# Kernel tuning notes

Hardware: AMD Instinct MI355X
Metric: run time of the kernel (lower is better)

Reference implementation:

```python
import jax, jax.numpy as jnp
import numpy as np

MAX_VISIT = 200
NUM_CODE = 506          # feature vocab -> 507 multi-hot dims
NUM_TGT = 284           # target vocab multi-hot dims
B = 64
P = 40                  # codes per visit
D_OTH = 57              # others feature dim (sign slice [37:] is 20-dim)
K = 100                 # len(weight_idx)
LSTM = 256
D_FEAT = (NUM_CODE + 1) + K + 27 + (D_OTH - 37)   # 654
D_FWD = D_FEAT + 10                                # 664
D_MLP_IN = (NUM_CODE + 1) + (D_OTH - 37) + 20 + 8  # 555


def multi_hot(codes, n):
    """Binary multi-hot encode int codes over last axis. codes: [..., P]."""
    shp = codes.shape
    flat = codes.reshape(-1, shp[-1])
    R = flat.shape[0]
    rows = jnp.repeat(jnp.arange(R), shp[-1])
    z = jnp.zeros((R, n), jnp.float32).at[rows, flat.reshape(-1)].set(1.0)
    return z.reshape(shp[:-1] + (n,))


def reverse_sequence(x, lengths):
    """tf.reverse_sequence along axis 1: reverse first lengths[i] steps, keep rest."""
    T = x.shape[1]
    j = jnp.arange(T)[None, :]
    L = lengths[:, None]
    idx = jnp.where(j < L, L - 1 - j, j)          # [B, T]
    return jnp.take_along_axis(x, idx[:, :, None], axis=1)


def setup_inputs() -> dict:
    key = jax.random.key(0)
    ks = jax.random.split(key, 13)
    code = jax.random.randint(ks[0], (B, MAX_VISIT, P), 0, NUM_CODE + 1, dtype=jnp.int32)
    others = jax.random.normal(ks[1], (B, MAX_VISIT, D_OTH), jnp.float32)
    length = jax.random.randint(ks[2], (B,), 3, MAX_VISIT + 1, dtype=jnp.int32)
    target = jax.random.randint(ks[3], (B, 10), 0, NUM_TGT, dtype=jnp.int32)
    weight_idx = jax.random.randint(ks[4], (K,), 0, NUM_TGT, dtype=jnp.int32)
    s = 0.02
    Wf = jax.random.normal(ks[5], (D_FWD, LSTM), jnp.float32) * s
    bf = jnp.zeros((LSTM,), jnp.float32)
    Wb = jax.random.normal(ks[6], (D_FWD, LSTM), jnp.float32) * s
    bb = jnp.zeros((LSTM,), jnp.float32)
    W0 = jax.random.normal(ks[7], (D_MLP_IN, 256), jnp.float32) * s
    b0 = jnp.zeros((256,), jnp.float32)
    W1 = jax.random.normal(ks[8], (256, 256), jnp.float32) * s
    b1 = jnp.zeros((256,), jnp.float32)
    return {"code": code, "others": others, "length": length, "target": target,
            "weight_idx": weight_idx, "Wf": Wf, "bf": bf, "Wb": Wb, "bb": bb,
            "W0": W0, "b0": b0, "W1": W1, "b1": b1}


def reference(code, others, length, target, weight_idx, Wf, bf, Wb, bb, W0, b0, W1, b1):
    code_mh = multi_hot(code, NUM_CODE + 1)                      # [B,200,507]
    # valid-visit mask (dense analogue of tf.boolean_mask over [B,198])
    mask = (jnp.arange(MAX_VISIT - 2)[None, :] < (length - 2)[:, None]).astype(jnp.float32)
    sign = others[:, 1:-1, 37:]                                  # [B,198,20]
    interval_ = jnp.concatenate([others[:, 1:-1, 27:37], others[:, 2:, 27:37]], axis=-1)
    stay = others[:, 1:-1, 19:27]
    x = jnp.concatenate([code_mh[:, 1:-1], sign, interval_, stay], axis=-1)  # [B,198,555]
    h = jax.nn.relu(x @ W0 + b0) @ W1 + b1                       # [B,198,256]
    fv = h / jnp.sqrt(jnp.sum(h * h, axis=-1, keepdims=True))
    fv = fv * mask[:, :, None]                                   # zero invalid rows
    # target block: gather (1 - multi-hot) at weight_idx, tile over visits
    tgt = 1.0 - multi_hot(target, NUM_TGT)                       # [B,284]
    tgt = tgt[:, weight_idx]                                     # [B,K]
    tgt = jnp.broadcast_to(tgt[:, None, :], (B, MAX_VISIT, K))
    code_full = jnp.concatenate([code_mh, tgt], axis=-1)         # [B,200,607]
    interval = others[:, :, 27:37]
    interval_backward = jnp.concatenate(
        [jnp.zeros((B, 1, 10), jnp.float32), reverse_sequence(interval, length)[:, :-1]], axis=1)
    feature = jnp.concatenate([code_full, others[:, :, :27], others[:, :, 37:]], axis=-1)
    feature_backward = reverse_sequence(feature, length)
    x_forward = jnp.concatenate([feature, interval], axis=-1)[:, :-2] @ Wf + bf
    x_backward = jnp.concatenate([feature_backward, interval_backward], axis=-1)[:, :-2] @ Wb + bb
    return (x_forward, x_backward, fv)
```

## Files before the change

### kernel.cpp

```cpp
#include <hip/hip_runtime.h>
#include <hip/hip_bf16.h>

typedef unsigned short u16;
typedef __attribute__((ext_vector_type(8))) short short8;
typedef __attribute__((ext_vector_type(4))) float f32x4;

#define TMAX 200
#define TOUT 198
#define PC 40
#define DOTH 57
#define NKT 9
#define FWD_OFF 0
#define BWD_OFF 3244032
#define FV_OFF  6488064
#define OWF 0
#define OWB 294912
#define OW0 589824
#define OW1 884736
#define OTF 1015808
#define OTB 1081344
#define WS_BYTES 1146880

__device__ __align__(16) unsigned char g_ws[WS_BYTES];

__device__ __forceinline__ u16 f2b(float v) {
  __hip_bfloat16 h = __float2bfloat16(v);
  return *(u16*)&h;
}

__global__ __launch_bounds__(256) void prep_kernel(
    const int* __restrict__ target, const int* __restrict__ widx,
    const float* __restrict__ Wf, const float* __restrict__ bfv,
    const float* __restrict__ Wb, const float* __restrict__ bbv,
    const float* __restrict__ W0, const float* __restrict__ W1)
{
  u16*   wsu = (u16*)g_ws;
  float* wsf = (float*)g_ws;
  int blk = blockIdx.x, n = threadIdx.x;
  if (blk < 248) {
    const float* src; u16* dst; int kb; int mode;
    if (blk < 72)       { src=Wf; dst=wsu+OWF/2; kb=blk;     mode=0; }
    else if (blk < 144) { src=Wb; dst=wsu+OWB/2; kb=blk-72;  mode=0; }
    else if (blk < 216) { src=W0; dst=wsu+OW0/2; kb=blk-144; mode=1; }
    else                { src=W1; dst=wsu+OW1/2; kb=blk-216; mode=2; }
    u16 pk[8];
    #pragma unroll
    for (int j=0;j<8;j++) {
      int k = kb*8+j;
      int sr;
      if (mode==0)      sr = (k<57)? 607+k : (k<564)? k-57 : -1;
      else if (mode==1) sr = (k<48)? 507+k : (k<57)? -1 : (k<564)? k-57 : -1;
      else              sr = k;
      float v = (sr>=0)? src[sr*256+n] : 0.f;
      pk[j] = f2b(v);
    }
    *(uint4*)(dst + (kb*256+n)*8) = *(uint4*)pk;
  } else {
    int b = blk - 248;
    __shared__ float tval[100]; __shared__ int tg[10];
    if (n<10) tg[n]=target[b*10+n];
    __syncthreads();
    if (n<100){ int w=widx[n]; float v=1.f;
      #pragma unroll
      for(int i=0;i<10;i++) if(tg[i]==w) v=0.f;
      tval[n]=v; }
    __syncthreads();
    float aF=bfv[n], aB=bbv[n];
    for(int k=0;k<100;k++){ float v=tval[k];
      aF=fmaf(v,Wf[(507+k)*256+n],aF); aB=fmaf(v,Wb[(507+k)*256+n],aB); }
    wsf[OTF/4 + b*256+n]=aF; wsf[OTB/4 + b*256+n]=aB;
  }
}

__global__ __launch_bounds__(256) void gemm_kernel(
    const int* __restrict__ code, const float* __restrict__ others,
    const int* __restrict__ length,
    const float* __restrict__ b0, const float* __restrict__ b1,
    float* __restrict__ out)
{
  const u16*   wsu = (const u16*)g_ws;
  const float* wsf = (const float*)g_ws;
  const int tile = blockIdx.x;
  const int strm = blockIdx.y;
  const int tid = threadIdx.x;
  const int wv = tid>>6, lane = tid&63, q = lane>>4, c = lane&15;
  const int colbase = wv*64 + c;

  __shared__ u16 lA[NKT*2048];
  __shared__ int rowB[32], rowT[32], rowS[32], rowS2[32], rowL[32];
  __shared__ float rpart[4][32];
  __shared__ int s_skip;

  if (tid == 0) s_skip = 1;
  if (tid < 32) {
    int m = tile*32 + tid;
    int b = m/198, t = m - b*198;
    int L = length[b];
    int s, s2 = 0;
    if (strm==0) s = t;
    else if (strm==1){ s = (t<L)? (L-1-t) : t;
                       s2 = (t==0)? -1 : (((t-1)<L)? (L-t) : (t-1)); }
    else s = t+1;
    rowB[tid]=b; rowT[tid]=t; rowS[tid]=s; rowS2[tid]=s2; rowL[tid]=L;
  }
  __syncthreads();

  if (strm == 2) {
    if (tid < 32 && rowT[tid] < rowL[tid]-2) s_skip = 0;
    __syncthreads();
    if (s_skip) {
      f32x4 z = {0.f, 0.f, 0.f, 0.f};
      #pragma unroll
      for (int it=0; it<8; it++) {
        int lin = it*256 + tid;
        int r = lin>>6, c4 = (lin&63)<<2;
        *(f32x4*)(out + FV_OFF + (rowB[r]*TOUT + rowT[r])*256 + c4) = z;
      }
      return;
    }
  }

  int myp[5], myr[5];
  #pragma unroll
  for (int it=0; it<5; it++) {
    int idx = tid + it*256;
    int r = idx/40, p = idx - r*40;
    myr[it] = r*8;
    myp[it] = 57 + code[(rowB[r]*TMAX + rowS[r])*PC + p];
  }

  float dv[8];
  if (strm < 2) {
    #pragma unroll
    for (int it=0; it<8; it++) {
      int idx = tid + it*256;
      float v = 0.f;
      if (idx < 32*57) {
        int r = idx/57, j = idx - r*57;
        int col = (j<27)? j : (j<47)? 37+(j-27) : 27+(j-47);
        int sr = (strm==1 && j>=47)? rowS2[r] : rowS[r];
        if (sr >= 0) v = others[(rowB[r]*TMAX + sr)*DOTH + col];
      }
      dv[it] = v;
    }
  } else {
    #pragma unroll
    for (int it=0; it<6; it++) {
      int idx = tid + it*256;
      int r = idx/48, j = idx - r*48;
      int t = rowT[r], srow, col;
      if (j<20)      { srow=t+1; col=37+j; }
      else if (j<30) { srow=t+1; col=27+(j-20); }
      else if (j<40) { srow=t+2; col=27+(j-30); }
      else           { srow=t+1; col=19+(j-40); }
      dv[it] = others[(rowB[r]*TMAX + srow)*DOTH + col];
    }
  }

  f32x4 acc[2][4];
  if (strm < 2) {
    const float* tg = wsf + ((strm==0)? OTF/4 : OTB/4);
    #pragma unroll
    for (int mt=0; mt<2; mt++)
      #pragma unroll
      for (int reg=0; reg<4; reg++) {
        int rl = mt*16 + q*4 + reg;
        const float* tr = tg + rowB[rl]*256;
        #pragma unroll
        for (int nt=0; nt<4; nt++) acc[mt][nt][reg] = tr[colbase + nt*16];
      }
  } else {
    #pragma unroll
    for (int nt=0; nt<4; nt++){ float v = b0[colbase + nt*16];
      #pragma unroll
      for (int mt=0; mt<2; mt++)
        #pragma unroll
        for (int reg=0; reg<4; reg++) acc[mt][nt][reg]=v; }
  }

  const u16* Wpk = wsu + ((strm==0)? OWF/2 : (strm==1)? OWB/2 : OW0/2);
  short8 bb[2][8];
  {
    const u16* gB0 = Wpk + ((q    )*256 + colbase)*8;
    const u16* gB1 = Wpk + ((4 + q)*256 + colbase)*8;
    #pragma unroll
    for (int nt=0; nt<4; nt++) {
      bb[0][nt]   = *(const short8*)(gB0 + nt*128);
      bb[0][nt+4] = *(const short8*)(gB1 + nt*128);
    }
  }

  { uint4 z = {0,0,0,0};
    #pragma unroll
    for (int i=0; i<NKT; i++) ((uint4*)lA)[tid + i*256] = z;
  }
  __syncthreads();
  #pragma unroll
  for (int it=0; it<5; it++) {
    int d = myp[it];
    lA[(d>>3)*256 + myr[it] + (d&7)] = 0x3F80;
  }
  if (strm < 2) {
    #pragma unroll
    for (int it=0; it<8; it++) {
      int idx = tid + it*256;
      if (idx < 32*57) {
        int r = idx/57, j = idx - r*57;
        lA[(j>>3)*256 + r*8 + (j&7)] = f2b(dv[it]);
      }
    }
  } else {
    #pragma unroll
    for (int it=0; it<6; it++) {
      int idx = tid + it*256;
      int r = idx/48, j = idx - r*48;
      lA[(j>>3)*256 + r*8 + (j&7)] = f2b(dv[it]);
    }
  }
  __syncthreads();

  #pragma unroll
  for (int kt=0; kt<NKT; kt++) {
    const u16* A = lA + kt*2048;
    short8 af0[2], af1[2];
    #pragma unroll
    for (int mt=0; mt<2; mt++) af0[mt] = *(const short8*)&A[(q    )*256 + (mt*16 + c)*8];
    #pragma unroll
    for (int mt=0; mt<2; mt++) af1[mt] = *(const short8*)&A[(4 + q)*256 + (mt*16 + c)*8];
    if (kt < NKT-1) {
      const u16* gB0 = Wpk + (((kt+1)*8 + q    )*256 + colbase)*8;
      const u16* gB1 = Wpk + (((kt+1)*8 + 4 + q)*256 + colbase)*8;
      #pragma unroll
      for (int nt=0; nt<4; nt++) {
        bb[(kt+1)&1][nt]   = *(const short8*)(gB0 + nt*128);
        bb[(kt+1)&1][nt+4] = *(const short8*)(gB1 + nt*128);
      }
    }
    #pragma unroll
    for (int mt=0; mt<2; mt++)
      #pragma unroll
      for (int nt=0; nt<4; nt++)
        acc[mt][nt] = __builtin_amdgcn_mfma_f32_16x16x32_bf16(af0[mt], bb[kt&1][nt], acc[mt][nt], 0,0,0);
    #pragma unroll
    for (int mt=0; mt<2; mt++)
      #pragma unroll
      for (int nt=0; nt<4; nt++)
        acc[mt][nt] = __builtin_amdgcn_mfma_f32_16x16x32_bf16(af1[mt], bb[kt&1][nt+4], acc[mt][nt], 0,0,0);
  }

  if (strm < 2) {
    float* o = out + ((strm==0)? FWD_OFF : BWD_OFF);
    #pragma unroll
    for (int mt=0; mt<2; mt++)
      #pragma unroll
      for (int reg=0; reg<4; reg++) {
        int rl = mt*16 + q*4 + reg;
        float* orow = o + (rowB[rl]*TOUT + rowT[rl])*256 + colbase;
        #pragma unroll
        for (int nt=0; nt<4; nt++) orow[nt*16] = acc[mt][nt][reg];
      }
  } else {
    __syncthreads();
    if (wv == 0) {
      #pragma unroll
      for (int mt=0; mt<2; mt++)
        #pragma unroll
        for (int reg=0; reg<4; reg++) {
          int rl = mt*16 + q*4 + reg;
          #pragma unroll
          for (int nt=0; nt<4; nt++) {
            int kl = c + nt*16;
            lA[(kl>>3)*256 + rl*8 + (kl&7)] = f2b(fmaxf(acc[mt][nt][reg], 0.f));
          }
        }
    }
    const u16* W1p = wsu + OW1/2;
    short8 bw[2][4];
    {
      const u16* gB = W1p + ((q)*256 + colbase)*8;
      #pragma unroll
      for (int nt=0; nt<4; nt++) bw[0][nt] = *(const short8*)(gB + nt*128);
    }
    __syncthreads();
    f32x4 a2[2][4];
    #pragma unroll
    for (int nt=0; nt<4; nt++){ float v = b1[colbase + nt*16];
      #pragma unroll
      for (int mt=0; mt<2; mt++)
        #pragma unroll
        for (int reg=0; reg<4; reg++) a2[mt][nt][reg]=v; }
    #pragma unroll
    for (int kt2=0; kt2<4; kt2++) {
      if (wv == kt2+1) {
        u16* B2 = lA + ((kt2+1)&1)*2048;
        #pragma unroll
        for (int mt=0; mt<2; mt++)
          #pragma unroll
          for (int reg=0; reg<4; reg++) {
            int rl = mt*16 + q*4 + reg;
            #pragma unroll
            for (int nt=0; nt<4; nt++) {
              int kl = c + nt*16;
              B2[(kl>>3)*256 + rl*8 + (kl&7)] = f2b(fmaxf(acc[mt][nt][reg], 0.f));
            }
          }
      }
      #pragma unroll
      for (int s=0; s<2; s++) {
        const int step = kt2*2 + s;
        const u16* A2 = lA + (kt2&1)*2048;
        int akb = s*4 + q;
        short8 af[2];
        #pragma unroll
        for (int mt=0; mt<2; mt++) af[mt] = *(const short8*)&A2[akb*256 + (mt*16 + c)*8];
        if (step < 7) {
          const int nstep = step + 1;
          const u16* gB = W1p + (((nstep>>1)*8 + (nstep&1)*4 + q)*256 + colbase)*8;
          #pragma unroll
          for (int nt=0; nt<4; nt++) bw[nstep&1][nt] = *(const short8*)(gB + nt*128);
        }
        #pragma unroll
        for (int mt=0; mt<2; mt++)
          #pragma unroll
          for (int nt=0; nt<4; nt++)
            a2[mt][nt] = __builtin_amdgcn_mfma_f32_16x16x32_bf16(af[mt], bw[step&1][nt], a2[mt][nt], 0,0,0);
      }
      __syncthreads();
    }
    #pragma unroll
    for (int mt=0; mt<2; mt++)
      #pragma unroll
      for (int reg=0; reg<4; reg++) {
        int rl = mt*16 + q*4 + reg;
        float ss = 0.f;
        #pragma unroll
        for (int nt=0; nt<4; nt++){ float v=a2[mt][nt][reg]; ss = fmaf(v,v,ss); }
        ss += __shfl_xor(ss, 1, 64); ss += __shfl_xor(ss, 2, 64);
        ss += __shfl_xor(ss, 4, 64); ss += __shfl_xor(ss, 8, 64);
        if (c==0) rpart[wv][rl] = ss;
      }
    __syncthreads();
    #pragma unroll
    for (int mt=0; mt<2; mt++)
      #pragma unroll
      for (int reg=0; reg<4; reg++) {
        int rl = mt*16 + q*4 + reg;
        float s = rpart[0][rl]+rpart[1][rl]+rpart[2][rl]+rpart[3][rl];
        float inv = (s>0.f)? (1.0f/sqrtf(s)) : 0.f;
        int t = rowT[rl];
        if (t >= rowL[rl]-2) inv = 0.f;
        float* orow = out + FV_OFF + (rowB[rl]*TOUT + t)*256 + colbase;
        #pragma unroll
        for (int nt=0; nt<4; nt++) orow[nt*16] = a2[mt][nt][reg]*inv;
      }
  }
}

extern "C" void kernel_launch(void* const* d_in, const int* in_sizes, int n_in,
                              void* d_out, int out_size, void* d_ws, size_t ws_size,
                              hipStream_t stream) {
  const int*   code    = (const int*)d_in[0];
  const float* others  = (const float*)d_in[1];
  const int*   length  = (const int*)d_in[2];
  const int*   target  = (const int*)d_in[3];
  const int*   widx    = (const int*)d_in[4];
  const float* Wf      = (const float*)d_in[5];
  const float* bfv     = (const float*)d_in[6];
  const float* Wb      = (const float*)d_in[7];
  const float* bbv     = (const float*)d_in[8];
  const float* W0      = (const float*)d_in[9];
  const float* b0v     = (const float*)d_in[10];
  const float* W1      = (const float*)d_in[11];
  const float* b1v     = (const float*)d_in[12];
  (void)d_ws; (void)ws_size;

  float* out = (float*)d_out;

  prep_kernel<<<dim3(312), dim3(256), 0, stream>>>(target, widx, Wf, bfv, Wb, bbv, W0, W1);
  gemm_kernel<<<dim3(396,3), dim3(256), 0, stream>>>(code, others, length, b0v, b1v, out);
}
```

Baseline: 124.6 us.

## Stage output tiles through LDS for vectorized stores and simplify MLP second layer

Accumulator outputs are first written to a padded LDS tile and then stored to global memory as contiguous 16-byte vectors, replacing scattered scalar stores. The second MLP layer now has every wave write its ReLU slice to LDS up front, followed by a plain non-unrolled K loop, instead of interleaving staged writes with barriers. Register double-buffering of weight prefetches is removed in favour of loads inside a non-unrolled loop, and launch bounds now request 4 blocks per CU. The goal is higher occupancy and store coalescing, at the cost of less explicit latency hiding for global weight loads and extra LDS round trips and barriers.

```diff
diff --git a/kernel.cpp b/kernel.cpp
--- a/kernel.cpp
+++ b/kernel.cpp
@@ -72,7 +72,7 @@
   }
 }
 
-__global__ __launch_bounds__(256) void gemm_kernel(
+__global__ __launch_bounds__(256, 4) void gemm_kernel(
     const int* __restrict__ code, const float* __restrict__ others,
     const int* __restrict__ length,
     const float* __restrict__ b0, const float* __restrict__ b1,
@@ -86,7 +86,7 @@
   const int wv = tid>>6, lane = tid&63, q = lane>>4, c = lane&15;
   const int colbase = wv*64 + c;
 
-  __shared__ u16 lA[NKT*2048];
+  __shared__ __align__(16) u16 lA[NKT*2048];
   __shared__ int rowB[32], rowT[32], rowS[32], rowS2[32], rowL[32];
   __shared__ float rpart[4][32];
   __shared__ int s_skip;
@@ -178,21 +178,9 @@
         for (int reg=0; reg<4; reg++) acc[mt][nt][reg]=v; }
   }
 
-  const u16* Wpk = wsu + ((strm==0)? OWF/2 : (strm==1)? OWB/2 : OW0/2);
-  short8 bb[2][8];
-  {
-    const u16* gB0 = Wpk + ((q    )*256 + colbase)*8;
-    const u16* gB1 = Wpk + ((4 + q)*256 + colbase)*8;
-    #pragma unroll
-    for (int nt=0; nt<4; nt++) {
-      bb[0][nt]   = *(const short8*)(gB0 + nt*128);
-      bb[0][nt+4] = *(const short8*)(gB1 + nt*128);
-    }
-  }
-
   { uint4 z = {0,0,0,0};
     #pragma unroll
-    for (int i=0; i<NKT; i++) ((uint4*)lA)[tid + i*256] = z;
+    for (int i=0; i<9; i++) ((uint4*)lA)[tid + i*256] = z;
   }
   __syncthreads();
   #pragma unroll
@@ -219,49 +207,58 @@
   }
   __syncthreads();
 
-  #pragma unroll
+  const u16* Wpk = wsu + ((strm==0)? OWF/2 : (strm==1)? OWB/2 : OW0/2);
+  #pragma unroll 1
   for (int kt=0; kt<NKT; kt++) {
+    const u16* gB0 = Wpk + ((kt*8 + q    )*256 + colbase)*8;
+    const u16* gB1 = Wpk + ((kt*8 + 4 + q)*256 + colbase)*8;
+    short8 bb[8];
+    #pragma unroll
+    for (int nt=0; nt<4; nt++) {
+      bb[nt]   = *(const short8*)(gB0 + nt*128);
+      bb[nt+4] = *(const short8*)(gB1 + nt*128);
+    }
     const u16* A = lA + kt*2048;
     short8 af0[2], af1[2];
     #pragma unroll
     for (int mt=0; mt<2; mt++) af0[mt] = *(const short8*)&A[(q    )*256 + (mt*16 + c)*8];
     #pragma unroll
     for (int mt=0; mt<2; mt++) af1[mt] = *(const short8*)&A[(4 + q)*256 + (mt*16 + c)*8];
-    if (kt < NKT-1) {
-      const u16* gB0 = Wpk + (((kt+1)*8 + q    )*256 + colbase)*8;
-      const u16* gB1 = Wpk + (((kt+1)*8 + 4 + q)*256 + colbase)*8;
-      #pragma unroll
-      for (int nt=0; nt<4; nt++) {
-        bb[(kt+1)&1][nt]   = *(const short8*)(gB0 + nt*128);
-        bb[(kt+1)&1][nt+4] = *(const short8*)(gB1 + nt*128);
-      }
-    }
     #pragma unroll
     for (int mt=0; mt<2; mt++)
       #pragma unroll
       for (int nt=0; nt<4; nt++)
-        acc[mt][nt] = __builtin_amdgcn_mfma_f32_16x16x32_bf16(af0[mt], bb[kt&1][nt], acc[mt][nt], 0,0,0);
+        acc[mt][nt] = __builtin_amdgcn_mfma_f32_16x16x32_bf16(af0[mt], bb[nt], acc[mt][nt], 0,0,0);
     #pragma unroll
     for (int mt=0; mt<2; mt++)
       #pragma unroll
       for (int nt=0; nt<4; nt++)
-        acc[mt][nt] = __builtin_amdgcn_mfma_f32_16x16x32_bf16(af1[mt], bb[kt&1][nt+4], acc[mt][nt], 0,0,0);
+        acc[mt][nt] = __builtin_amdgcn_mfma_f32_16x16x32_bf16(af1[mt], bb[nt+4], acc[mt][nt], 0,0,0);
   }
 
   if (strm < 2) {
-    float* o = out + ((strm==0)? FWD_OFF : BWD_OFF);
+    __syncthreads();
+    float* fC = (float*)lA;
     #pragma unroll
     for (int mt=0; mt<2; mt++)
       #pragma unroll
       for (int reg=0; reg<4; reg++) {
         int rl = mt*16 + q*4 + reg;
-        float* orow = o + (rowB[rl]*TOUT + rowT[rl])*256 + colbase;
-        #pragma unroll
-        for (int nt=0; nt<4; nt++) orow[nt*16] = acc[mt][nt][reg];
-      }
-  } else {
-    __syncthreads();
-    if (wv == 0) {
+        #pragma unroll
+        for (int nt=0; nt<4; nt++) fC[rl*260 + colbase + nt*16] = acc[mt][nt][reg];
+      }
+    __syncthreads();
+    float* o = out + ((strm==0)? FWD_OFF : BWD_OFF);
+    #pragma unroll
+    for (int it=0; it<8; it++) {
+      int row = it*4 + (tid>>6), col = (tid&63)*4;
+      f32x4 v = *(f32x4*)&fC[row*260 + col];
+      *(f32x4*)(o + (rowB[row]*TOUT + rowT[row])*256 + col) = v;
+    }
+  } else {
+    __syncthreads();
+    {
+      u16* B2 = lA + wv*2048;
       #pragma unroll
       for (int mt=0; mt<2; mt++)
         #pragma unroll
@@ -270,62 +267,36 @@
           #pragma unroll
           for (int nt=0; nt<4; nt++) {
             int kl = c + nt*16;
-            lA[(kl>>3)*256 + rl*8 + (kl&7)] = f2b(fmaxf(acc[mt][nt][reg], 0.f));
+            B2[(kl>>3)*256 + rl*8 + (kl&7)] = f2b(fmaxf(acc[mt][nt][reg], 0.f));
           }
         }
     }
+    __syncthreads();
+    f32x4 a2[2][4];
+    #pragma unroll
+    for (int nt=0; nt<4; nt++){ float v = b1[colbase + nt*16];
+      #pragma unroll
+      for (int mt=0; mt<2; mt++)
+        #pragma unroll
+        for (int reg=0; reg<4; reg++) a2[mt][nt][reg]=v; }
     const u16* W1p = wsu + OW1/2;
-    short8 bw[2][4];
-    {
-      const u16* gB = W1p + ((q)*256 + colbase)*8;
-      #pragma unroll
-      for (int nt=0; nt<4; nt++) bw[0][nt] = *(const short8*)(gB + nt*128);
-    }
-    __syncthreads();
-    f32x4 a2[2][4];
-    #pragma unroll
-    for (int nt=0; nt<4; nt++){ float v = b1[colbase + nt*16];
+    #pragma unroll 1
+    for (int step=0; step<8; step++) {
+      int kt2 = step>>1;
+      int akb = (step&1)*4 + q;
+      const u16* gB = W1p + ((kt2*8 + akb)*256 + colbase)*8;
+      short8 bf[4];
+      #pragma unroll
+      for (int nt=0; nt<4; nt++) bf[nt] = *(const short8*)(gB + nt*128);
+      const u16* A2 = lA + kt2*2048;
+      short8 af[2];
+      #pragma unroll
+      for (int mt=0; mt<2; mt++) af[mt] = *(const short8*)&A2[akb*256 + (mt*16 + c)*8];
       #pragma unroll
       for (int mt=0; mt<2; mt++)
         #pragma unroll
-        for (int reg=0; reg<4; reg++) a2[mt][nt][reg]=v; }
-    #pragma unroll
-    for (int kt2=0; kt2<4; kt2++) {
-      if (wv == kt2+1) {
-        u16* B2 = lA + ((kt2+1)&1)*2048;
-        #pragma unroll
-        for (int mt=0; mt<2; mt++)
-          #pragma unroll
-          for (int reg=0; reg<4; reg++) {
-            int rl = mt*16 + q*4 + reg;
-            #pragma unroll
-            for (int nt=0; nt<4; nt++) {
-              int kl = c + nt*16;
-              B2[(kl>>3)*256 + rl*8 + (kl&7)] = f2b(fmaxf(acc[mt][nt][reg], 0.f));
-            }
-          }
-      }
-      #pragma unroll
-      for (int s=0; s<2; s++) {
-        const int step = kt2*2 + s;
-        const u16* A2 = lA + (kt2&1)*2048;
-        int akb = s*4 + q;
-        short8 af[2];
-        #pragma unroll
-        for (int mt=0; mt<2; mt++) af[mt] = *(const short8*)&A2[akb*256 + (mt*16 + c)*8];
-        if (step < 7) {
-          const int nstep = step + 1;
-          const u16* gB = W1p + (((nstep>>1)*8 + (nstep&1)*4 + q)*256 + colbase)*8;
-          #pragma unroll
-          for (int nt=0; nt<4; nt++) bw[nstep&1][nt] = *(const short8*)(gB + nt*128);
-        }
-        #pragma unroll
-        for (int mt=0; mt<2; mt++)
-          #pragma unroll
-          for (int nt=0; nt<4; nt++)
-            a2[mt][nt] = __builtin_amdgcn_mfma_f32_16x16x32_bf16(af[mt], bw[step&1][nt], a2[mt][nt], 0,0,0);
-      }
-      __syncthreads();
+        for (int nt=0; nt<4; nt++)
+          a2[mt][nt] = __builtin_amdgcn_mfma_f32_16x16x32_bf16(af[mt], bf[nt], a2[mt][nt], 0,0,0);
     }
     #pragma unroll
     for (int mt=0; mt<2; mt++)
@@ -340,6 +311,7 @@
         if (c==0) rpart[wv][rl] = ss;
       }
     __syncthreads();
+    float* fC = (float*)lA;
     #pragma unroll
     for (int mt=0; mt<2; mt++)
       #pragma unroll
@@ -347,12 +319,17 @@
         int rl = mt*16 + q*4 + reg;
         float s = rpart[0][rl]+rpart[1][rl]+rpart[2][rl]+rpart[3][rl];
         float inv = (s>0.f)? (1.0f/sqrtf(s)) : 0.f;
-        int t = rowT[rl];
-        if (t >= rowL[rl]-2) inv = 0.f;
-        float* orow = out + FV_OFF + (rowB[rl]*TOUT + t)*256 + colbase;
-        #pragma unroll
-        for (int nt=0; nt<4; nt++) orow[nt*16] = a2[mt][nt][reg]*inv;
-      }
+        if (rowT[rl] >= rowL[rl]-2) inv = 0.f;
+        #pragma unroll
+        for (int nt=0; nt<4; nt++) fC[rl*260 + colbase + nt*16] = a2[mt][nt][reg]*inv;
+      }
+    __syncthreads();
+    #pragma unroll
+    for (int it=0; it<8; it++) {
+      int row = it*4 + (tid>>6), col = (tid&63)*4;
+      f32x4 v = *(f32x4*)&fC[row*260 + col];
+      *(f32x4*)(out + FV_OFF + (rowB[row]*TOUT + rowT[row])*256 + col) = v;
+    }
   }
 }
 
```

Result: no change. 122.9 us (-1.4%).

## Retile LSTM-input GEMM to 64x128 blocks with rolling 3-slot LDS A buffer

Applied to the files above, without the earlier changes.

The forward/backward projection GEMMs now use 64-row by 128-column tiles (grid 198x2x3) instead of 32-row by full-width tiles. The A operand is built per 64-wide K chunk in a rotating three-buffer LDS ring rather than materialising all nine K tiles up front. The MLP stream keeps 32-row tiles, chosen by the half index, and uses the same rolling buffer. The goal is to shrink LDS usage for higher occupancy (launch_bounds 256,3) and to overlap zeroing and scattering of the multi-hot A with the MFMAs, at the cost of a barrier per K step and fewer weight columns reused per block.

```diff
diff --git a/kernel.cpp b/kernel.cpp
--- a/kernel.cpp
+++ b/kernel.cpp
@@ -66,13 +66,14 @@
       tval[n]=v; }
     __syncthreads();
     float aF=bfv[n], aB=bbv[n];
+    #pragma unroll 4
     for(int k=0;k<100;k++){ float v=tval[k];
       aF=fmaf(v,Wf[(507+k)*256+n],aF); aB=fmaf(v,Wb[(507+k)*256+n],aB); }
     wsf[OTF/4 + b*256+n]=aF; wsf[OTB/4 + b*256+n]=aB;
   }
 }
 
-__global__ __launch_bounds__(256) void gemm_kernel(
+__global__ __launch_bounds__(256, 3) void gemm_kernel(
     const int* __restrict__ code, const float* __restrict__ others,
     const int* __restrict__ length,
     const float* __restrict__ b0, const float* __restrict__ b1,
@@ -81,19 +82,19 @@
   const u16*   wsu = (const u16*)g_ws;
   const float* wsf = (const float*)g_ws;
   const int tile = blockIdx.x;
-  const int strm = blockIdx.y;
+  const int half = blockIdx.y;
+  const int strm = blockIdx.z;
   const int tid = threadIdx.x;
   const int wv = tid>>6, lane = tid&63, q = lane>>4, c = lane&15;
-  const int colbase = wv*64 + c;
-
-  __shared__ u16 lA[NKT*2048];
-  __shared__ int rowB[32], rowT[32], rowS[32], rowS2[32], rowL[32];
-  __shared__ float rpart[4][32];
+
+  __shared__ __align__(16) u16 lA[3][4096];
+  __shared__ int rowB[64], rowT[64], rowS[64], rowS2[64], rowL[64];
+  __shared__ float rpart[4][64];
   __shared__ int s_skip;
 
   if (tid == 0) s_skip = 1;
-  if (tid < 32) {
-    int m = tile*32 + tid;
+  if (tid < 64) {
+    int m = tile*64 + tid;
     int b = m/198, t = m - b*198;
     int L = length[b];
     int s, s2 = 0;
@@ -105,37 +106,24 @@
   }
   __syncthreads();
 
-  if (strm == 2) {
-    if (tid < 32 && rowT[tid] < rowL[tid]-2) s_skip = 0;
-    __syncthreads();
-    if (s_skip) {
-      f32x4 z = {0.f, 0.f, 0.f, 0.f};
-      #pragma unroll
-      for (int it=0; it<8; it++) {
-        int lin = it*256 + tid;
-        int r = lin>>6, c4 = (lin&63)<<2;
-        *(f32x4*)(out + FV_OFF + (rowB[r]*TOUT + rowT[r])*256 + c4) = z;
-      }
-      return;
-    }
-  }
-
-  int myp[5], myr[5];
-  #pragma unroll
-  for (int it=0; it<5; it++) {
-    int idx = tid + it*256;
-    int r = idx/40, p = idx - r*40;
-    myr[it] = r*8;
-    myp[it] = 57 + code[(rowB[r]*TMAX + rowS[r])*PC + p];
-  }
-
-  float dv[8];
   if (strm < 2) {
-    #pragma unroll
-    for (int it=0; it<8; it++) {
+    const int colbase = half*128 + wv*32 + c;
+
+    int myp[10], myr[10];
+    #pragma unroll
+    for (int it=0; it<10; it++) {
+      int idx = tid + it*256;
+      int r = idx/40, p = idx - r*40;
+      myr[it] = r*8;
+      myp[it] = 57 + code[(rowB[r]*TMAX + rowS[r])*PC + p];
+    }
+
+    float dv[15];
+    #pragma unroll
+    for (int it=0; it<15; it++) {
       int idx = tid + it*256;
       float v = 0.f;
-      if (idx < 32*57) {
+      if (idx < 3648) {
         int r = idx/57, j = idx - r*57;
         int col = (j<27)? j : (j<47)? 37+(j-27) : 27+(j-47);
         int sr = (strm==1 && j>=47)? rowS2[r] : rowS[r];
@@ -143,124 +131,216 @@
       }
       dv[it] = v;
     }
+
+    f32x4 acc[4][2];
+    {
+      const float* tg = wsf + ((strm==0)? OTF/4 : OTB/4);
+      #pragma unroll
+      for (int mt=0; mt<4; mt++)
+        #pragma unroll
+        for (int reg=0; reg<4; reg++) {
+          int rl = mt*16 + q*4 + reg;
+          const float* tr = tg + rowB[rl]*256;
+          #pragma unroll
+          for (int nt=0; nt<2; nt++) acc[mt][nt][reg] = tr[colbase + nt*16];
+        }
+    }
+
+    const u16* Wpk = wsu + ((strm==0)? OWF/2 : OWB/2);
+    short8 bb[2][4];
+    #pragma unroll
+    for (int kb=0; kb<2; kb++) {
+      const u16* gB = Wpk + ((kb*4 + q)*256 + colbase)*8;
+      #pragma unroll
+      for (int nt=0; nt<2; nt++) bb[0][kb*2+nt] = *(const short8*)(gB + nt*128);
+    }
+
+    { uint4 z = {0,0,0,0};
+      ((uint4*)lA[0])[tid] = z; ((uint4*)lA[0])[tid+256] = z;
+      ((uint4*)lA[1])[tid] = z; ((uint4*)lA[1])[tid+256] = z; }
+    __syncthreads();
+    #pragma unroll
+    for (int it=0; it<10; it++) {
+      unsigned d = (unsigned)(myp[it]);
+      if (d < 64u) lA[0][(d>>3)*512 + myr[it] + (d&7)] = 0x3F80;
+    }
+    #pragma unroll
+    for (int it=0; it<15; it++) {
+      int idx = tid + it*256;
+      if (idx < 3648) {
+        int r = idx/57, j = idx - r*57;
+        lA[0][(j>>3)*512 + r*8 + (j&7)] = f2b(dv[it]);
+      }
+    }
+    __syncthreads();
+
+    #pragma unroll
+    for (int kt=0; kt<NKT; kt++) {
+      const u16* A = lA[kt%3];
+      short8 af0[4], af1[4];
+      #pragma unroll
+      for (int mt=0; mt<4; mt++) af0[mt] = *(const short8*)&A[(q    )*512 + (mt*16 + c)*8];
+      #pragma unroll
+      for (int mt=0; mt<4; mt++) af1[mt] = *(const short8*)&A[(4 + q)*512 + (mt*16 + c)*8];
+      if (kt < NKT-1) {
+        #pragma unroll
+        for (int kb=0; kb<2; kb++) {
+          const u16* gB = Wpk + (((kt+1)*8 + kb*4 + q)*256 + colbase)*8;
+          #pragma unroll
+          for (int nt=0; nt<2; nt++) bb[(kt+1)&1][kb*2+nt] = *(const short8*)(gB + nt*128);
+        }
+        u16* nb = lA[(kt+1)%3];
+        const int k0n = (kt+1)*64;
+        #pragma unroll
+        for (int it=0; it<10; it++) {
+          unsigned d = (unsigned)(myp[it] - k0n);
+          if (d < 64u) nb[(d>>3)*512 + myr[it] + (d&7)] = 0x3F80;
+        }
+      }
+      if (kt < NKT-2) {
+        uint4 z = {0,0,0,0};
+        ((uint4*)lA[(kt+2)%3])[tid] = z; ((uint4*)lA[(kt+2)%3])[tid+256] = z;
+      }
+      #pragma unroll
+      for (int mt=0; mt<4; mt++)
+        #pragma unroll
+        for (int nt=0; nt<2; nt++)
+          acc[mt][nt] = __builtin_amdgcn_mfma_f32_16x16x32_bf16(af0[mt], bb[kt&1][nt], acc[mt][nt], 0,0,0);
+      #pragma unroll
+      for (int mt=0; mt<4; mt++)
+        #pragma unroll
+        for (int nt=0; nt<2; nt++)
+          acc[mt][nt] = __builtin_amdgcn_mfma_f32_16x16x32_bf16(af1[mt], bb[kt&1][2+nt], acc[mt][nt], 0,0,0);
+      __syncthreads();
+    }
+
+    float* o = out + ((strm==0)? FWD_OFF : BWD_OFF);
+    #pragma unroll
+    for (int mt=0; mt<4; mt++)
+      #pragma unroll
+      for (int reg=0; reg<4; reg++) {
+        int rl = mt*16 + q*4 + reg;
+        float* orow = o + (rowB[rl]*TOUT + rowT[rl])*256 + colbase;
+        #pragma unroll
+        for (int nt=0; nt<2; nt++) orow[nt*16] = acc[mt][nt][reg];
+      }
   } else {
+    const int mo = half*32;
+    const int colbase = wv*64 + c;
+    u16* w32 = (u16*)lA;
+
+    if (tid < 32 && rowT[mo+tid] < rowL[mo+tid]-2) s_skip = 0;
+    __syncthreads();
+    if (s_skip) {
+      f32x4 z = {0.f, 0.f, 0.f, 0.f};
+      #pragma unroll
+      for (int it=0; it<8; it++) {
+        int lin = it*256 + tid;
+        int r = mo + (lin>>6), c4 = (lin&63)<<2;
+        *(f32x4*)(out + FV_OFF + (rowB[r]*TOUT + rowT[r])*256 + c4) = z;
+      }
+      return;
+    }
+
+    int myp[5], myr[5];
+    #pragma unroll
+    for (int it=0; it<5; it++) {
+      int idx = tid + it*256;
+      int r = idx/40, p = idx - r*40;
+      myr[it] = r*8;
+      myp[it] = 57 + code[(rowB[mo+r]*TMAX + rowS[mo+r])*PC + p];
+    }
+
+    float dv[6];
     #pragma unroll
     for (int it=0; it<6; it++) {
       int idx = tid + it*256;
       int r = idx/48, j = idx - r*48;
-      int t = rowT[r], srow, col;
+      int t = rowT[mo+r], srow, col;
       if (j<20)      { srow=t+1; col=37+j; }
       else if (j<30) { srow=t+1; col=27+(j-20); }
       else if (j<40) { srow=t+2; col=27+(j-30); }
       else           { srow=t+1; col=19+(j-40); }
-      dv[it] = others[(rowB[r]*TMAX + srow)*DOTH + col];
-    }
-  }
-
-  f32x4 acc[2][4];
-  if (strm < 2) {
-    const float* tg = wsf + ((strm==0)? OTF/4 : OTB/4);
-    #pragma unroll
-    for (int mt=0; mt<2; mt++)
-      #pragma unroll
-      for (int reg=0; reg<4; reg++) {
-        int rl = mt*16 + q*4 + reg;
-        const float* tr = tg + rowB[rl]*256;
-        #pragma unroll
-        for (int nt=0; nt<4; nt++) acc[mt][nt][reg] = tr[colbase + nt*16];
-      }
-  } else {
+      dv[it] = others[(rowB[mo+r]*TMAX + srow)*DOTH + col];
+    }
+
+    f32x4 acc[2][4];
     #pragma unroll
     for (int nt=0; nt<4; nt++){ float v = b0[colbase + nt*16];
       #pragma unroll
       for (int mt=0; mt<2; mt++)
         #pragma unroll
         for (int reg=0; reg<4; reg++) acc[mt][nt][reg]=v; }
-  }
-
-  const u16* Wpk = wsu + ((strm==0)? OWF/2 : (strm==1)? OWB/2 : OW0/2);
-  short8 bb[2][8];
-  {
-    const u16* gB0 = Wpk + ((q    )*256 + colbase)*8;
-    const u16* gB1 = Wpk + ((4 + q)*256 + colbase)*8;
-    #pragma unroll
-    for (int nt=0; nt<4; nt++) {
-      bb[0][nt]   = *(const short8*)(gB0 + nt*128);
-      bb[0][nt+4] = *(const short8*)(gB1 + nt*128);
-    }
-  }
-
-  { uint4 z = {0,0,0,0};
-    #pragma unroll
-    for (int i=0; i<NKT; i++) ((uint4*)lA)[tid + i*256] = z;
-  }
-  __syncthreads();
-  #pragma unroll
-  for (int it=0; it<5; it++) {
-    int d = myp[it];
-    lA[(d>>3)*256 + myr[it] + (d&7)] = 0x3F80;
-  }
-  if (strm < 2) {
-    #pragma unroll
-    for (int it=0; it<8; it++) {
-      int idx = tid + it*256;
-      if (idx < 32*57) {
-        int r = idx/57, j = idx - r*57;
-        lA[(j>>3)*256 + r*8 + (j&7)] = f2b(dv[it]);
-      }
-    }
-  } else {
+
+    const u16* Wpk = wsu + OW0/2;
+    short8 bb[2][8];
+    {
+      const u16* gB0 = Wpk + ((q    )*256 + colbase)*8;
+      const u16* gB1 = Wpk + ((4 + q)*256 + colbase)*8;
+      #pragma unroll
+      for (int nt=0; nt<4; nt++) {
+        bb[0][nt]   = *(const short8*)(gB0 + nt*128);
+        bb[0][nt+4] = *(const short8*)(gB1 + nt*128);
+      }
+    }
+
+    { uint4 z = {0,0,0,0};
+      ((uint4*)w32)[tid] = z; ((uint4*)w32)[tid+256] = z; }
+    __syncthreads();
+    #pragma unroll
+    for (int it=0; it<5; it++) {
+      unsigned d = (unsigned)(myp[it]);
+      if (d < 64u) w32[(d>>3)*256 + myr[it] + (d&7)] = 0x3F80;
+    }
     #pragma unroll
     for (int it=0; it<6; it++) {
       int idx = tid + it*256;
       int r = idx/48, j = idx - r*48;
-      lA[(j>>3)*256 + r*8 + (j&7)] = f2b(dv[it]);
-    }
-  }
-  __syncthreads();
-
-  #pragma unroll
-  for (int kt=0; kt<NKT; kt++) {
-    const u16* A = lA + kt*2048;
-    short8 af0[2], af1[2];
-    #pragma unroll
-    for (int mt=0; mt<2; mt++) af0[mt] = *(const short8*)&A[(q    )*256 + (mt*16 + c)*8];
-    #pragma unroll
-    for (int mt=0; mt<2; mt++) af1[mt] = *(const short8*)&A[(4 + q)*256 + (mt*16 + c)*8];
-    if (kt < NKT-1) {
-      const u16* gB0 = Wpk + (((kt+1)*8 + q    )*256 + colbase)*8;
-      const u16* gB1 = Wpk + (((kt+1)*8 + 4 + q)*256 + colbase)*8;
-      #pragma unroll
-      for (int nt=0; nt<4; nt++) {
-        bb[(kt+1)&1][nt]   = *(const short8*)(gB0 + nt*128);
-        bb[(kt+1)&1][nt+4] = *(const short8*)(gB1 + nt*128);
-      }
-    }
-    #pragma unroll
-    for (int mt=0; mt<2; mt++)
-      #pragma unroll
-      for (int nt=0; nt<4; nt++)
-        acc[mt][nt] = __builtin_amdgcn_mfma_f32_16x16x32_bf16(af0[mt], bb[kt&1][nt], acc[mt][nt], 0,0,0);
-    #pragma unroll
-    for (int mt=0; mt<2; mt++)
-      #pragma unroll
-      for (int nt=0; nt<4; nt++)
-        acc[mt][nt] = __builtin_amdgcn_mfma_f32_16x16x32_bf16(af1[mt], bb[kt&1][nt+4], acc[mt][nt], 0,0,0);
-  }
-
-  if (strm < 2) {
-    float* o = out + ((strm==0)? FWD_OFF : BWD_OFF);
-    #pragma unroll
-    for (int mt=0; mt<2; mt++)
-      #pragma unroll
-      for (int reg=0; reg<4; reg++) {
-        int rl = mt*16 + q*4 + reg;
-        float* orow = o + (rowB[rl]*TOUT + rowT[rl])*256 + colbase;
-        #pragma unroll
-        for (int nt=0; nt<4; nt++) orow[nt*16] = acc[mt][nt][reg];
-      }
-  } else {
-    __syncthreads();
+      w32[(j>>3)*256 + r*8 + (j&7)] = f2b(dv[it]);
+    }
+    __syncthreads();
+
+    #pragma unroll
+    for (int kt=0; kt<NKT; kt++) {
+      const u16* A = w32 + (kt%3)*2048;
+      short8 af0[2], af1[2];
+      #pragma unroll
+      for (int mt=0; mt<2; mt++) af0[mt] = *(const short8*)&A[(q    )*256 + (mt*16 + c)*8];
+      #pragma unroll
+      for (int mt=0; mt<2; mt++) af1[mt] = *(const short8*)&A[(4 + q)*256 + (mt*16 + c)*8];
+      if (kt < NKT-1) {
+        const u16* gB0 = Wpk + (((kt+1)*8 + q    )*256 + colbase)*8;
+        const u16* gB1 = Wpk + (((kt+1)*8 + 4 + q)*256 + colbase)*8;
+        #pragma unroll
+        for (int nt=0; nt<4; nt++) {
+          bb[(kt+1)&1][nt]   = *(const short8*)(gB0 + nt*128);
+          bb[(kt+1)&1][nt+4] = *(const short8*)(gB1 + nt*128);
+        }
+        u16* nb = w32 + ((kt+1)%3)*2048;
+        const int k0n = (kt+1)*64;
+        #pragma unroll
+        for (int it=0; it<5; it++) {
+          unsigned d = (unsigned)(myp[it] - k0n);
+          if (d < 64u) nb[(d>>3)*256 + myr[it] + (d&7)] = 0x3F80;
+        }
+      }
+      if (kt < NKT-2) {
+        uint4 z = {0,0,0,0};
+        ((uint4*)(w32 + ((kt+2)%3)*2048))[tid] = z;
+      }
+      #pragma unroll
+      for (int mt=0; mt<2; mt++)
+        #pragma unroll
+        for (int nt=0; nt<4; nt++)
+          acc[mt][nt] = __builtin_amdgcn_mfma_f32_16x16x32_bf16(af0[mt], bb[kt&1][nt], acc[mt][nt], 0,0,0);
+      #pragma unroll
+      for (int mt=0; mt<2; mt++)
+        #pragma unroll
+        for (int nt=0; nt<4; nt++)
+          acc[mt][nt] = __builtin_amdgcn_mfma_f32_16x16x32_bf16(af1[mt], bb[kt&1][nt+4], acc[mt][nt], 0,0,0);
+      __syncthreads();
+    }
+
     if (wv == 0) {
       #pragma unroll
       for (int mt=0; mt<2; mt++)
@@ -270,7 +350,7 @@
           #pragma unroll
           for (int nt=0; nt<4; nt++) {
             int kl = c + nt*16;
-            lA[(kl>>3)*256 + rl*8 + (kl&7)] = f2b(fmaxf(acc[mt][nt][reg], 0.f));
+            w32[(kl>>3)*256 + rl*8 + (kl&7)] = f2b(fmaxf(acc[mt][nt][reg], 0.f));
           }
         }
     }
@@ -292,7 +372,7 @@
     #pragma unroll
     for (int kt2=0; kt2<4; kt2++) {
       if (wv == kt2+1) {
-        u16* B2 = lA + ((kt2+1)&1)*2048;
+        u16* B2 = w32 + ((kt2+1)&1)*2048;
         #pragma unroll
         for (int mt=0; mt<2; mt++)
           #pragma unroll
@@ -308,7 +388,7 @@
       #pragma unroll
       for (int s=0; s<2; s++) {
         const int step = kt2*2 + s;
-        const u16* A2 = lA + (kt2&1)*2048;
+        const u16* A2 = w32 + (kt2&1)*2048;
         int akb = s*4 + q;
         short8 af[2];
         #pragma unroll
@@ -347,9 +427,9 @@
         int rl = mt*16 + q*4 + reg;
         float s = rpart[0][rl]+rpart[1][rl]+rpart[2][rl]+rpart[3][rl];
         float inv = (s>0.f)? (1.0f/sqrtf(s)) : 0.f;
-        int t = rowT[rl];
-        if (t >= rowL[rl]-2) inv = 0.f;
-        float* orow = out + FV_OFF + (rowB[rl]*TOUT + t)*256 + colbase;
+        int t = rowT[mo+rl];
+        if (t >= rowL[mo+rl]-2) inv = 0.f;
+        float* orow = out + FV_OFF + (rowB[mo+rl]*TOUT + t)*256 + colbase;
         #pragma unroll
         for (int nt=0; nt<4; nt++) orow[nt*16] = a2[mt][nt][reg]*inv;
       }
@@ -377,5 +457,5 @@
   float* out = (float*)d_out;
 
   prep_kernel<<<dim3(312), dim3(256), 0, stream>>>(target, widx, Wf, bfv, Wb, bbv, W0, W1);
-  gemm_kernel<<<dim3(396,3), dim3(256), 0, stream>>>(code, others, length, b0v, b1v, out);
+  gemm_kernel<<<dim3(198,2,3), dim3(256), 0, stream>>>(code, others, length, b0v, b1v, out);
 }
```

After: 130.2 us. 4.5% more time.
